# Kernel tuning notes

Measured on AMD Instinct MI355X. Metric: run time of the kernel, lower is better.

The kernel has to match this reference:

```python
import jax, jax.numpy as jnp
import numpy as np

E = 1024
H = 16
D = E // H  # head dim


def setup_inputs() -> dict:
    key = jax.random.key(0)
    ks = jax.random.split(key, 8)
    N, L = 4, 2048
    x = jax.random.normal(ks[0], (N, L, E), dtype=jnp.float32)
    attn_mask = jnp.zeros((N, L), dtype=jnp.float32)  # additive mask
    s = 0.02
    Wq = jax.random.normal(ks[1], (E, E), dtype=jnp.float32) * s
    bq = jnp.zeros((E,), dtype=jnp.float32)
    Wk = jax.random.normal(ks[2], (E, E), dtype=jnp.float32) * s
    bk = jnp.zeros((E,), dtype=jnp.float32)
    Wv = jax.random.normal(ks[3], (E, E), dtype=jnp.float32) * s
    bv = jnp.zeros((E,), dtype=jnp.float32)
    return {"x": x, "attn_mask": attn_mask, "Wq": Wq, "bq": bq,
            "Wk": Wk, "bk": bk, "Wv": Wv, "bv": bv}


def _to_heads(t):
    N, L, _ = t.shape
    return t.reshape(N, L, H, D).transpose(0, 2, 1, 3)  # [N,H,L,D]


def reference(x, attn_mask, Wq, bq, Wk, bk, Wv, bv):
    # Linear projections (torch Linear: x @ W.T + b)
    Q = _to_heads(x @ Wq.T + bq) * (1.0 / jnp.sqrt(jnp.float32(D)))
    K = _to_heads(x @ Wk.T + bk)
    V = _to_heads(x @ Wv.T + bv)
    scores = jnp.einsum('nhqd,nhkd->nhqk', Q, K) + attn_mask[:, None, None, :]
    attn = jax.nn.softmax(scores, axis=-1)  # dropout p=0 -> identity
    out = jnp.einsum('nhqk,nhkd->nhqd', attn, V)  # [N,H,L,D]
    N, _, L, _ = out.shape
    return out.transpose(0, 2, 1, 3).reshape(N, L, E)
```

## Files before the change

### kernel.cpp

```cpp
#include <hip/hip_runtime.h>

#define DEV __device__ __forceinline__

typedef unsigned short u16;
typedef __attribute__((ext_vector_type(8))) __bf16 bf16x8;
typedef __attribute__((ext_vector_type(4))) float f32x4;
typedef __attribute__((ext_vector_type(16))) float f32x16;

#define LOG2E 1.44269504088896340736f

DEV u16 f2bf(float f) {
  union { float f; unsigned u; } v; v.f = f;
  unsigned r = v.u + 0x7FFFu + ((v.u >> 16) & 1u);
  return (u16)(r >> 16);
}

DEV float exp2_fast(float x) {
#if __has_builtin(__builtin_amdgcn_exp2f)
  return __builtin_amdgcn_exp2f(x);
#else
  float r;
  asm volatile("v_exp_f32 %0, %1" : "=v"(r) : "v"(x));
  return r;
#endif
}

DEV float xor32_f(float v) { return __shfl_xor(v, 32, 64); }
DEV unsigned xor32_u(unsigned v) {
  return (unsigned)__shfl_xor((int)v, 32, 64);
}
DEV unsigned cvtpk(float lo, float hi) {
  unsigned r;
  asm volatile("v_cvt_pk_bf16_f32 %0, %1, %2" : "=v"(r) : "v"(lo), "v"(hi));
  return r;
}
DEV float bperm_f(int srclane, float v) {
  union { float f; int i; } u;
  u.f = v;
  u.i = __builtin_amdgcn_ds_bpermute(srclane * 4, u.i);
  return u.f;
}

template <typename T>
DEV void gload_lds16(const T* g, T* l) {
  __builtin_amdgcn_global_load_lds(
      (const __attribute__((address_space(1))) void*)(g),
      (__attribute__((address_space(3))) void*)(l),
      16, 0, 0);
}

DEV bf16x8 ldfrag(const u16* p) { return *(const bf16x8*)p; }

DEV void cast8(const float* __restrict__ in, u16* __restrict__ out) {
  float4 a = ((const float4*)in)[0];
  float4 b = ((const float4*)in)[1];
  uint4 o;
  o.x = (unsigned)f2bf(a.x) | ((unsigned)f2bf(a.y) << 16);
  o.y = (unsigned)f2bf(a.z) | ((unsigned)f2bf(a.w) << 16);
  o.z = (unsigned)f2bf(b.x) | ((unsigned)f2bf(b.y) << 16);
  o.w = (unsigned)f2bf(b.z) | ((unsigned)f2bf(b.w) << 16);
  *(uint4*)out = o;
}

__global__ __launch_bounds__(256) void prep_kernel(
    const float* __restrict__ x, const float* __restrict__ Wq,
    const float* __restrict__ Wk, const float* __restrict__ Wv,
    const float* __restrict__ mask,
    u16* __restrict__ xb, u16* __restrict__ wb, float* __restrict__ mlog) {
  const int i = blockIdx.x * 256 + threadIdx.x;
  const int NX = 8192 * 1024 / 8;
  const int NW = 1024 * 1024 / 8;
  if (i < NX) {
    cast8(x + (long)i * 8, xb + (long)i * 8);
  } else if (i < NX + 3 * NW) {
    int j = i - NX;
    int sel = j / NW;
    int jj = j - sel * NW;
    const float* W = (sel == 0) ? Wq : (sel == 1) ? Wk : Wv;
    cast8(W + (long)jj * 8, wb + (long)j * 8);
  } else {
    int j = i - NX - 3 * NW;
    float4 a = ((const float4*)mask)[2 * j];
    float4 b = ((const float4*)mask)[2 * j + 1];
    a.x *= LOG2E; a.y *= LOG2E; a.z *= LOG2E; a.w *= LOG2E;
    b.x *= LOG2E; b.y *= LOG2E; b.z *= LOG2E; b.w *= LOG2E;
    ((float4*)mlog)[2 * j] = a;
    ((float4*)mlog)[2 * j + 1] = b;
  }
}

__global__ __launch_bounds__(256) void qkv_gemm(
    const u16* __restrict__ xb, const u16* __restrict__ wb,
    const float* __restrict__ bq, const float* __restrict__ bk, const float* __restrict__ bv,
    u16* __restrict__ qb, u16* __restrict__ kb, u16* __restrict__ vtb) {
  __shared__ u16 As[128 * 64];
  __shared__ u16 Bs[128 * 64];
  const int t = threadIdx.x, lane = t & 63, w = t >> 6;
  const int wm = w >> 1, wn = w & 1;
  const int m0 = blockIdx.x * 128;
  const int cb = blockIdx.y;
  const int wsel = cb >> 3;
  const int n0 = (cb & 7) * 128;
  const u16* W = wb + wsel * (1024 * 1024);
  const float* bias = (wsel == 0) ? bq : (wsel == 1) ? bk : bv;
  const float scale = (wsel == 0) ? 0.125f * LOG2E : 1.0f;

  f32x4 acc[4][4];
  const f32x4 z4 = {0.f, 0.f, 0.f, 0.f};
  for (int i = 0; i < 4; ++i)
    for (int j = 0; j < 4; ++j) acc[i][j] = z4;

  const int srow = w * 32 + (lane >> 3);
  const int scol = (lane & 7) * 8;

  for (int k0 = 0; k0 < 1024; k0 += 64) {
    __syncthreads();
    for (int i = 0; i < 4; ++i) {
      gload_lds16(xb + (m0 + srow + i * 8) * 1024 + k0 + scol, &As[w * 2048 + i * 512]);
      gload_lds16(W + (n0 + srow + i * 8) * 1024 + k0 + scol, &Bs[w * 2048 + i * 512]);
    }
    __syncthreads();
    for (int ks = 0; ks < 2; ++ks) {
      bf16x8 a[4], b[4];
      for (int mi = 0; mi < 4; ++mi)
        a[mi] = ldfrag(&As[(wm * 64 + mi * 16 + (lane & 15)) * 64 + ks * 32 + (lane >> 4) * 8]);
      for (int ni = 0; ni < 4; ++ni)
        b[ni] = ldfrag(&Bs[(wn * 64 + ni * 16 + (lane & 15)) * 64 + ks * 32 + (lane >> 4) * 8]);
      for (int mi = 0; mi < 4; ++mi)
        for (int ni = 0; ni < 4; ++ni)
          acc[mi][ni] = __builtin_amdgcn_mfma_f32_16x16x32_bf16(a[mi], b[ni], acc[mi][ni], 0, 0, 0);
    }
  }
  if (wsel == 2) {
    for (int ni = 0; ni < 4; ++ni) {
      int col = n0 + wn * 64 + ni * 16 + (lane & 15);
      float bv_ = bias[col];
      int h = col >> 6, d = col & 63;
      for (int mi = 0; mi < 4; ++mi) {
        int gm = m0 + wm * 64 + mi * 16 + (lane >> 4) * 4;
        int nn = gm >> 11, lq = gm & 2047;
        ushort4 pk;
        pk.x = f2bf(acc[mi][ni][0] + bv_);
        pk.y = f2bf(acc[mi][ni][1] + bv_);
        pk.z = f2bf(acc[mi][ni][2] + bv_);
        pk.w = f2bf(acc[mi][ni][3] + bv_);
        *(ushort4*)(vtb + ((long)((nn << 4) + h) * 64 + d) * 2048 + lq) = pk;
      }
    }
  } else {
    u16* dst = (wsel == 0) ? qb : kb;
    for (int ni = 0; ni < 4; ++ni) {
      int col = n0 + wn * 64 + ni * 16 + (lane & 15);
      float bv_ = bias[col];
      int h = col >> 6, d = col & 63;
      for (int mi = 0; mi < 4; ++mi) {
        for (int r = 0; r < 4; ++r) {
          int gm = m0 + wm * 64 + mi * 16 + (lane >> 4) * 4 + r;
          int nn = gm >> 11, lq = gm & 2047;
          float val = acc[mi][ni][r] * scale + bv_;
          dst[(((nn << 4) + h) * 2048 + lq) * 64 + d] = f2bf(val);
        }
      }
    }
  }
}

__global__ __launch_bounds__(256) void flash_attn(
    const u16* __restrict__ qb, const u16* __restrict__ kb, const u16* __restrict__ vtb,
    const float* __restrict__ mlog, float* __restrict__ out) {
  __shared__ u16 SM[4][64 * 64];
  __shared__ float MK[2048];

  const int t = threadIdx.x, lane = t & 63, w = t >> 6;
  const int hi = lane >> 5, l31 = lane & 31;
  const int bid = blockIdx.x;
  const int swz = (bid & 7) * 128 + (bid >> 3);
  const int q0 = (swz & 15) * 128;
  const int head = swz >> 4;
  const int n = head >> 4, h = head & 15;

  const u16* qh = qb + head * (2048 * 64);
  const u16* kh = kb + head * (2048 * 64);
  const u16* vth = vtb + head * (64 * 2048);
  const float* mrow = mlog + n * 2048;

  const int srow8 = lane >> 3;
  const int scolsw = ((lane & 7) ^ srow8) * 8;
  const int rsw = (lane & 7) * 8;
  int fcolB[4];
  for (int dk = 0; dk < 4; ++dk) fcolB[dk] = (16 * dk + 8 * hi) ^ rsw;

  u16* QL = &SM[0][0];
  for (int i = 0; i < 4; ++i)
    gload_lds16(qh + (q0 + w * 32 + i * 8 + srow8) * 64 + scolsw, &QL[(w * 32 + i * 8) * 64]);
  for (int i = 0; i < 2; ++i) {
    int chunk = w * 2 + i;
    gload_lds16(mrow + chunk * 256 + lane * 4, &MK[chunk * 256]);
  }
  __syncthreads();
  bf16x8 qf[4];
  for (int dk = 0; dk < 4; ++dk)
    qf[dk] = ldfrag(&QL[(w * 32 + l31) * 64 + fcolB[dk]]);
  __syncthreads();

  {
    gload_lds16(kh + (w * 16 + srow8) * 64 + scolsw, &SM[0][w * 1024]);
    gload_lds16(kh + (w * 16 + 8 + srow8) * 64 + scolsw, &SM[0][w * 1024 + 512]);
    for (int i = 0; i < 2; ++i) {
      int dbase = w * 16 + i * 8;
      gload_lds16(vth + (dbase + srow8) * 2048 + scolsw, &SM[2][dbase * 64]);
    }
  }

  f32x16 o0, o1;
  for (int r = 0; r < 16; ++r) { o0[r] = 0.f; o1[r] = 0.f; }
  float m_ = -1e30f, lp = 0.f;

  for (int tt = 0; tt < 32; ++tt) {
    const int cur = tt & 1;
    const int kv0 = tt * 64;
    __syncthreads();

    if (tt < 31) {
      const int kv1 = kv0 + 64;
      const u16* ksrc = kh + kv1 * 64;
      gload_lds16(ksrc + (w * 16 + srow8) * 64 + scolsw, &SM[cur ^ 1][w * 1024]);
      gload_lds16(ksrc + (w * 16 + 8 + srow8) * 64 + scolsw, &SM[cur ^ 1][w * 1024 + 512]);
      for (int i = 0; i < 2; ++i) {
        int dbase = w * 16 + i * 8;
        gload_lds16(vth + (dbase + srow8) * 2048 + kv1 + scolsw, &SM[2 + (cur ^ 1)][dbase * 64]);
      }
    }
    const u16* Kc = &SM[cur][0];
    const u16* Vc = &SM[2 + cur][0];

    f32x16 s1, s2;
    {
      const float* mb = &MK[kv0 + 4 * hi];
      for (int mq = 0; mq < 4; ++mq) {
        f32x4 ma = *(const f32x4*)(mb + 8 * mq);
        f32x4 mc = *(const f32x4*)(mb + 32 + 8 * mq);
        for (int e = 0; e < 4; ++e) { s1[4 * mq + e] = ma[e]; s2[4 * mq + e] = mc[e]; }
      }
    }
    __builtin_amdgcn_s_setprio(1);
    for (int dk = 0; dk < 4; ++dk) {
      bf16x8 k0 = ldfrag(&Kc[l31 * 64 + fcolB[dk]]);
      bf16x8 k1 = ldfrag(&Kc[(32 + l31) * 64 + fcolB[dk]]);
      s1 = __builtin_amdgcn_mfma_f32_32x32x16_bf16(k0, qf[dk], s1, 0, 0, 0);
      s2 = __builtin_amdgcn_mfma_f32_32x32x16_bf16(k1, qf[dk], s2, 0, 0, 0);
    }
    __builtin_amdgcn_s_setprio(0);

    float tm[16];
#pragma unroll
    for (int r = 0; r < 16; ++r) tm[r] = fmaxf(s1[r], s2[r]);
#pragma unroll
    for (int st = 8; st >= 1; st >>= 1)
#pragma unroll
      for (int r = 0; r < st; ++r) tm[r] = fmaxf(tm[r], tm[r + st]);
    float pml = tm[0];

    if (!__all(pml <= m_ + 8.f)) {
      float pm = fmaxf(pml, xor32_f(pml));
      float nm = fmaxf(m_, pm);
      float sc = exp2_fast(m_ - nm);
      m_ = nm;
      lp *= sc;
      for (int r = 0; r < 16; ++r) {
        float scr = bperm_f((r & 3) + 8 * (r >> 2) + 4 * hi, sc);
        o0[r] *= scr;
        o1[r] *= scr;
      }
    }

#pragma unroll
    for (int r = 0; r < 16; ++r) {
      s1[r] = exp2_fast(s1[r] - m_);
      s2[r] = exp2_fast(s2[r] - m_);
    }
    float ts[16];
#pragma unroll
    for (int r = 0; r < 16; ++r) ts[r] = s1[r] + s2[r];
#pragma unroll
    for (int st = 8; st >= 1; st >>= 1)
#pragma unroll
      for (int r = 0; r < st; ++r) ts[r] += ts[r + st];
    lp += ts[0];

    unsigned raw[16];
#pragma unroll
    for (int mq = 0; mq < 8; ++mq) {
      raw[mq] = cvtpk(s1[2 * mq], s1[2 * mq + 1]);
      raw[8 + mq] = cvtpk(s2[2 * mq], s2[2 * mq + 1]);
    }
    union { unsigned u[16]; bf16x8 v[4]; } pw;
#pragma unroll
    for (int g = 0; g < 4; ++g) {
      unsigned a0 = raw[4 * g], a1 = raw[4 * g + 1];
      unsigned a2 = raw[4 * g + 2], a3 = raw[4 * g + 3];
      unsigned v0 = hi ? a0 : a2;
      unsigned v1 = hi ? a1 : a3;
      unsigned x0 = xor32_u(v0);
      unsigned x1 = xor32_u(v1);
      pw.u[4 * g + 0] = hi ? x0 : a0;
      pw.u[4 * g + 1] = hi ? x1 : a1;
      pw.u[4 * g + 2] = hi ? a2 : x0;
      pw.u[4 * g + 3] = hi ? a3 : x1;
    }

    __builtin_amdgcn_s_setprio(1);
    for (int kc = 0; kc < 4; ++kc) {
      bf16x8 bv0 = ldfrag(&Vc[l31 * 64 + fcolB[kc]]);
      bf16x8 bv1 = ldfrag(&Vc[(32 + l31) * 64 + fcolB[kc]]);
      o0 = __builtin_amdgcn_mfma_f32_32x32x16_bf16(pw.v[kc], bv0, o0, 0, 0, 0);
      o1 = __builtin_amdgcn_mfma_f32_32x32x16_bf16(pw.v[kc], bv1, o1, 0, 0, 0);
    }
    __builtin_amdgcn_s_setprio(0);
  }

  float lpf = lp + xor32_f(lp);
  float inv = 1.0f / lpf;
  for (int r = 0; r < 16; ++r) {
    int qrow = (r & 3) + 8 * (r >> 2) + 4 * hi;
    float invr = bperm_f(qrow, inv);
    int q = q0 + w * 32 + qrow;
    float* ob = out + (n * 2048 + q) * 1024 + h * 64;
    ob[l31] = o0[r] * invr;
    ob[32 + l31] = o1[r] * invr;
  }
}

extern "C" void kernel_launch(void* const* d_in, const int* in_sizes, int n_in,
                              void* d_out, int out_size, void* d_ws, size_t ws_size,
                              hipStream_t stream) {
  const float* x = (const float*)d_in[0];
  const float* mask = (const float*)d_in[1];
  const float* Wq = (const float*)d_in[2];
  const float* bq = (const float*)d_in[3];
  const float* Wk = (const float*)d_in[4];
  const float* bk = (const float*)d_in[5];
  const float* Wv = (const float*)d_in[6];
  const float* bv = (const float*)d_in[7];
  float* out = (float*)d_out;

  u16* xb = (u16*)d_ws;
  u16* wb = xb + 8192 * 1024;
  u16* qb = wb + 3 * 1024 * 1024;
  u16* kb = qb + 64 * 2048 * 64;
  u16* vtb = kb + 64 * 2048 * 64;
  float* mlog = (float*)(vtb + 64 * 2048 * 64);

  prep_kernel<<<1442816 / 256, 256, 0, stream>>>(x, Wq, Wk, Wv, mask, xb, wb, mlog);
  qkv_gemm<<<dim3(64, 24), 256, 0, stream>>>(xb, wb, bq, bk, bv, qb, kb, vtb);
  flash_attn<<<1024, 256, 0, stream>>>(qb, kb, vtb, mlog, out);
}
```

Baseline: 207.5 us.

## Process two 32-row query tiles per wave in flash attention to reuse K/V fragments

Each wave now handles 64 query rows, as two independent 32-row sub-tiles, so every block covers 256 queries and the grid shrinks from 1024 to 512 blocks. Each K and V fragment read from LDS now feeds twice as many MFMAs, and the K/V global-to-LDS traffic per query is halved. The cost is roughly double the accumulator and score registers per wave, which may lower occupancy or cause spills. On a 256-CU part, 512 blocks is also only two blocks per CU, which hurts load balance.

```diff
diff --git a/kernel.cpp b/kernel.cpp
--- a/kernel.cpp
+++ b/kernel.cpp
@@ -174,9 +174,9 @@
   const int t = threadIdx.x, lane = t & 63, w = t >> 6;
   const int hi = lane >> 5, l31 = lane & 31;
   const int bid = blockIdx.x;
-  const int swz = (bid & 7) * 128 + (bid >> 3);
-  const int q0 = (swz & 15) * 128;
-  const int head = swz >> 4;
+  const int swz = (bid & 7) * 64 + (bid >> 3);
+  const int q0 = (swz & 7) * 256;
+  const int head = swz >> 3;
   const int n = head >> 4, h = head & 15;
 
   const u16* qh = qb + head * (2048 * 64);
@@ -191,16 +191,18 @@
   for (int dk = 0; dk < 4; ++dk) fcolB[dk] = (16 * dk + 8 * hi) ^ rsw;
 
   u16* QL = &SM[0][0];
-  for (int i = 0; i < 4; ++i)
-    gload_lds16(qh + (q0 + w * 32 + i * 8 + srow8) * 64 + scolsw, &QL[(w * 32 + i * 8) * 64]);
+  for (int i = 0; i < 8; ++i)
+    gload_lds16(qh + (q0 + w * 64 + i * 8 + srow8) * 64 + scolsw, &QL[(w * 64 + i * 8) * 64]);
   for (int i = 0; i < 2; ++i) {
     int chunk = w * 2 + i;
     gload_lds16(mrow + chunk * 256 + lane * 4, &MK[chunk * 256]);
   }
   __syncthreads();
-  bf16x8 qf[4];
-  for (int dk = 0; dk < 4; ++dk)
-    qf[dk] = ldfrag(&QL[(w * 32 + l31) * 64 + fcolB[dk]]);
+  bf16x8 qfA[4], qfB[4];
+  for (int dk = 0; dk < 4; ++dk) {
+    qfA[dk] = ldfrag(&QL[(w * 64 + l31) * 64 + fcolB[dk]]);
+    qfB[dk] = ldfrag(&QL[(w * 64 + 32 + l31) * 64 + fcolB[dk]]);
+  }
   __syncthreads();
 
   {
@@ -212,9 +214,10 @@
     }
   }
 
-  f32x16 o0, o1;
-  for (int r = 0; r < 16; ++r) { o0[r] = 0.f; o1[r] = 0.f; }
-  float m_ = -1e30f, lp = 0.f;
+  f32x16 o0A, o1A, o0B, o1B;
+  for (int r = 0; r < 16; ++r) { o0A[r] = 0.f; o1A[r] = 0.f; o0B[r] = 0.f; o1B[r] = 0.f; }
+  float mA = -1e30f, lpA = 0.f;
+  float mB = -1e30f, lpB = 0.f;
 
   for (int tt = 0; tt < 32; ++tt) {
     const int cur = tt & 1;
@@ -234,100 +237,149 @@
     const u16* Kc = &SM[cur][0];
     const u16* Vc = &SM[2 + cur][0];
 
-    f32x16 s1, s2;
+    f32x16 s1A, s2A, s1B, s2B;
     {
       const float* mb = &MK[kv0 + 4 * hi];
       for (int mq = 0; mq < 4; ++mq) {
         f32x4 ma = *(const f32x4*)(mb + 8 * mq);
         f32x4 mc = *(const f32x4*)(mb + 32 + 8 * mq);
-        for (int e = 0; e < 4; ++e) { s1[4 * mq + e] = ma[e]; s2[4 * mq + e] = mc[e]; }
+        for (int e = 0; e < 4; ++e) {
+          s1A[4 * mq + e] = ma[e]; s2A[4 * mq + e] = mc[e];
+          s1B[4 * mq + e] = ma[e]; s2B[4 * mq + e] = mc[e];
+        }
       }
     }
     __builtin_amdgcn_s_setprio(1);
     for (int dk = 0; dk < 4; ++dk) {
       bf16x8 k0 = ldfrag(&Kc[l31 * 64 + fcolB[dk]]);
       bf16x8 k1 = ldfrag(&Kc[(32 + l31) * 64 + fcolB[dk]]);
-      s1 = __builtin_amdgcn_mfma_f32_32x32x16_bf16(k0, qf[dk], s1, 0, 0, 0);
-      s2 = __builtin_amdgcn_mfma_f32_32x32x16_bf16(k1, qf[dk], s2, 0, 0, 0);
+      s1A = __builtin_amdgcn_mfma_f32_32x32x16_bf16(k0, qfA[dk], s1A, 0, 0, 0);
+      s2A = __builtin_amdgcn_mfma_f32_32x32x16_bf16(k1, qfA[dk], s2A, 0, 0, 0);
+      s1B = __builtin_amdgcn_mfma_f32_32x32x16_bf16(k0, qfB[dk], s1B, 0, 0, 0);
+      s2B = __builtin_amdgcn_mfma_f32_32x32x16_bf16(k1, qfB[dk], s2B, 0, 0, 0);
     }
     __builtin_amdgcn_s_setprio(0);
 
-    float tm[16];
-#pragma unroll
-    for (int r = 0; r < 16; ++r) tm[r] = fmaxf(s1[r], s2[r]);
+    float tmA[16], tmB[16];
+#pragma unroll
+    for (int r = 0; r < 16; ++r) {
+      tmA[r] = fmaxf(s1A[r], s2A[r]);
+      tmB[r] = fmaxf(s1B[r], s2B[r]);
+    }
 #pragma unroll
     for (int st = 8; st >= 1; st >>= 1)
 #pragma unroll
-      for (int r = 0; r < st; ++r) tm[r] = fmaxf(tm[r], tm[r + st]);
-    float pml = tm[0];
-
-    if (!__all(pml <= m_ + 8.f)) {
-      float pm = fmaxf(pml, xor32_f(pml));
-      float nm = fmaxf(m_, pm);
-      float sc = exp2_fast(m_ - nm);
-      m_ = nm;
-      lp *= sc;
+      for (int r = 0; r < st; ++r) {
+        tmA[r] = fmaxf(tmA[r], tmA[r + st]);
+        tmB[r] = fmaxf(tmB[r], tmB[r + st]);
+      }
+    float pmlA = tmA[0], pmlB = tmB[0];
+
+    int ok = (pmlA <= mA + 8.f) && (pmlB <= mB + 8.f);
+    if (!__all(ok)) {
+      float pmA = fmaxf(pmlA, xor32_f(pmlA));
+      float pmB = fmaxf(pmlB, xor32_f(pmlB));
+      float nmA = fmaxf(mA, pmA), nmB = fmaxf(mB, pmB);
+      float scA = exp2_fast(mA - nmA), scB = exp2_fast(mB - nmB);
+      mA = nmA; mB = nmB;
+      lpA *= scA; lpB *= scB;
       for (int r = 0; r < 16; ++r) {
-        float scr = bperm_f((r & 3) + 8 * (r >> 2) + 4 * hi, sc);
-        o0[r] *= scr;
-        o1[r] *= scr;
+        int qrow = (r & 3) + 8 * (r >> 2) + 4 * hi;
+        float srA = bperm_f(qrow, scA);
+        float srB = bperm_f(qrow, scB);
+        o0A[r] *= srA; o1A[r] *= srA;
+        o0B[r] *= srB; o1B[r] *= srB;
       }
     }
 
 #pragma unroll
     for (int r = 0; r < 16; ++r) {
-      s1[r] = exp2_fast(s1[r] - m_);
-      s2[r] = exp2_fast(s2[r] - m_);
-    }
-    float ts[16];
-#pragma unroll
-    for (int r = 0; r < 16; ++r) ts[r] = s1[r] + s2[r];
+      s1A[r] = exp2_fast(s1A[r] - mA);
+      s2A[r] = exp2_fast(s2A[r] - mA);
+      s1B[r] = exp2_fast(s1B[r] - mB);
+      s2B[r] = exp2_fast(s2B[r] - mB);
+    }
+    float tsA[16], tsB[16];
+#pragma unroll
+    for (int r = 0; r < 16; ++r) {
+      tsA[r] = s1A[r] + s2A[r];
+      tsB[r] = s1B[r] + s2B[r];
+    }
 #pragma unroll
     for (int st = 8; st >= 1; st >>= 1)
 #pragma unroll
-      for (int r = 0; r < st; ++r) ts[r] += ts[r + st];
-    lp += ts[0];
-
-    unsigned raw[16];
+      for (int r = 0; r < st; ++r) {
+        tsA[r] += tsA[r + st];
+        tsB[r] += tsB[r + st];
+      }
+    lpA += tsA[0];
+    lpB += tsB[0];
+
+    unsigned rawA[16], rawB[16];
 #pragma unroll
     for (int mq = 0; mq < 8; ++mq) {
-      raw[mq] = cvtpk(s1[2 * mq], s1[2 * mq + 1]);
-      raw[8 + mq] = cvtpk(s2[2 * mq], s2[2 * mq + 1]);
-    }
-    union { unsigned u[16]; bf16x8 v[4]; } pw;
+      rawA[mq] = cvtpk(s1A[2 * mq], s1A[2 * mq + 1]);
+      rawA[8 + mq] = cvtpk(s2A[2 * mq], s2A[2 * mq + 1]);
+      rawB[mq] = cvtpk(s1B[2 * mq], s1B[2 * mq + 1]);
+      rawB[8 + mq] = cvtpk(s2B[2 * mq], s2B[2 * mq + 1]);
+    }
+    union { unsigned u[16]; bf16x8 v[4]; } pwA, pwB;
 #pragma unroll
     for (int g = 0; g < 4; ++g) {
-      unsigned a0 = raw[4 * g], a1 = raw[4 * g + 1];
-      unsigned a2 = raw[4 * g + 2], a3 = raw[4 * g + 3];
-      unsigned v0 = hi ? a0 : a2;
-      unsigned v1 = hi ? a1 : a3;
-      unsigned x0 = xor32_u(v0);
-      unsigned x1 = xor32_u(v1);
-      pw.u[4 * g + 0] = hi ? x0 : a0;
-      pw.u[4 * g + 1] = hi ? x1 : a1;
-      pw.u[4 * g + 2] = hi ? a2 : x0;
-      pw.u[4 * g + 3] = hi ? a3 : x1;
+      {
+        unsigned a0 = rawA[4 * g], a1 = rawA[4 * g + 1];
+        unsigned a2 = rawA[4 * g + 2], a3 = rawA[4 * g + 3];
+        unsigned v0 = hi ? a0 : a2;
+        unsigned v1 = hi ? a1 : a3;
+        unsigned x0 = xor32_u(v0);
+        unsigned x1 = xor32_u(v1);
+        pwA.u[4 * g + 0] = hi ? x0 : a0;
+        pwA.u[4 * g + 1] = hi ? x1 : a1;
+        pwA.u[4 * g + 2] = hi ? a2 : x0;
+        pwA.u[4 * g + 3] = hi ? a3 : x1;
+      }
+      {
+        unsigned a0 = rawB[4 * g], a1 = rawB[4 * g + 1];
+        unsigned a2 = rawB[4 * g + 2], a3 = rawB[4 * g + 3];
+        unsigned v0 = hi ? a0 : a2;
+        unsigned v1 = hi ? a1 : a3;
+        unsigned x0 = xor32_u(v0);
+        unsigned x1 = xor32_u(v1);
+        pwB.u[4 * g + 0] = hi ? x0 : a0;
+        pwB.u[4 * g + 1] = hi ? x1 : a1;
+        pwB.u[4 * g + 2] = hi ? a2 : x0;
+        pwB.u[4 * g + 3] = hi ? a3 : x1;
+      }
     }
 
     __builtin_amdgcn_s_setprio(1);
     for (int kc = 0; kc < 4; ++kc) {
       bf16x8 bv0 = ldfrag(&Vc[l31 * 64 + fcolB[kc]]);
       bf16x8 bv1 = ldfrag(&Vc[(32 + l31) * 64 + fcolB[kc]]);
-      o0 = __builtin_amdgcn_mfma_f32_32x32x16_bf16(pw.v[kc], bv0, o0, 0, 0, 0);
-      o1 = __builtin_amdgcn_mfma_f32_32x32x16_bf16(pw.v[kc], bv1, o1, 0, 0, 0);
+      o0A = __builtin_amdgcn_mfma_f32_32x32x16_bf16(pwA.v[kc], bv0, o0A, 0, 0, 0);
+      o1A = __builtin_amdgcn_mfma_f32_32x32x16_bf16(pwA.v[kc], bv1, o1A, 0, 0, 0);
+      o0B = __builtin_amdgcn_mfma_f32_32x32x16_bf16(pwB.v[kc], bv0, o0B, 0, 0, 0);
+      o1B = __builtin_amdgcn_mfma_f32_32x32x16_bf16(pwB.v[kc], bv1, o1B, 0, 0, 0);
     }
     __builtin_amdgcn_s_setprio(0);
   }
 
-  float lpf = lp + xor32_f(lp);
-  float inv = 1.0f / lpf;
+  float lpfA = lpA + xor32_f(lpA);
+  float lpfB = lpB + xor32_f(lpB);
+  float invA = 1.0f / lpfA;
+  float invB = 1.0f / lpfB;
   for (int r = 0; r < 16; ++r) {
     int qrow = (r & 3) + 8 * (r >> 2) + 4 * hi;
-    float invr = bperm_f(qrow, inv);
-    int q = q0 + w * 32 + qrow;
-    float* ob = out + (n * 2048 + q) * 1024 + h * 64;
-    ob[l31] = o0[r] * invr;
-    ob[32 + l31] = o1[r] * invr;
+    float irA = bperm_f(qrow, invA);
+    float irB = bperm_f(qrow, invB);
+    int qA = q0 + w * 64 + qrow;
+    int qB = qA + 32;
+    float* obA = out + (n * 2048 + qA) * 1024 + h * 64;
+    float* obB = out + (n * 2048 + qB) * 1024 + h * 64;
+    obA[l31] = o0A[r] * irA;
+    obA[32 + l31] = o1A[r] * irA;
+    obB[l31] = o0B[r] * irB;
+    obB[32 + l31] = o1B[r] * irB;
   }
 }
 
@@ -353,5 +405,5 @@
 
   prep_kernel<<<1442816 / 256, 256, 0, stream>>>(x, Wq, Wk, Wv, mask, xb, wb, mlog);
   qkv_gemm<<<dim3(64, 24), 256, 0, stream>>>(xb, wb, bq, bk, bv, qb, kb, vtb);
-  flash_attn<<<1024, 256, 0, stream>>>(qb, kb, vtb, mlog, out);
-}
+  flash_attn<<<512, 256, 0, stream>>>(qb, kb, vtb, mlog, out);
+}
```

After: 248.2 us. 19.6% more time.
